# Optimization experiments

Hardware: AMD Instinct MI355X
Metric: run time of the kernel (lower is better)

Reference implementation:

```python
import jax, jax.numpy as jnp
import numpy as np

H = 1024
EPS = 1e-5
MIX_SCALE = 0.1


def setup_inputs() -> dict:
    key = jax.random.key(0)
    ks = jax.random.split(key, 6)
    B, S = 8, 4096
    x = jax.random.normal(ks[0], (B, S, H), dtype=jnp.float32)
    # to_complex: Linear(H, 2H); store weight as [H, 2H] for x @ W
    W_to = jax.random.normal(ks[1], (H, 2 * H), dtype=jnp.float32) * (1.0 / np.sqrt(H))
    b_to = jax.random.normal(ks[2], (2 * H,), dtype=jnp.float32) * 0.01
    # from_complex: Linear(2H, H)
    W_from = jax.random.normal(ks[3], (2 * H, H), dtype=jnp.float32) * (1.0 / np.sqrt(2 * H))
    b_from = jax.random.normal(ks[4], (H,), dtype=jnp.float32) * 0.01
    phase_shifts = jnp.zeros((1, 1, H), dtype=jnp.float32)
    return {"x": x, "W_to": W_to, "b_to": b_to, "W_from": W_from,
            "b_from": b_from, "phase_shifts": phase_shifts}


def reference(x, W_to, b_to, W_from, b_from, phase_shifts):
    # x: [B,S,H]
    complex_repr = x @ W_to + b_to                      # [B,S,2H]
    real, imag = jnp.split(complex_repr, 2, axis=-1)    # each [B,S,H]
    magnitude = jnp.sqrt(real**2 + imag**2 + EPS)
    phase = jnp.arctan2(imag, real)                     # [B,S,H]
    # mean_j cos(phase_i - phase_j + shift)
    #   = cos(phase_i + shift) * mean_j cos(phase_j)
    #   + sin(phase_i + shift) * mean_j sin(phase_j)
    # (exact trig identity; replaces the [B,S,S,H] materialization)
    mean_cos = jnp.mean(jnp.cos(phase), axis=1, keepdims=True)  # [B,1,H]
    mean_sin = jnp.mean(jnp.sin(phase), axis=1, keepdims=True)  # [B,1,H]
    shifted = phase + phase_shifts                              # [B,S,H]
    mixed_phase = jnp.cos(shifted) * mean_cos + jnp.sin(shifted) * mean_sin
    new_phase = phase + mixed_phase * MIX_SCALE
    new_real = magnitude * jnp.cos(new_phase)
    new_imag = magnitude * jnp.sin(new_phase)
    new_complex = jnp.concatenate([new_real, new_imag], axis=-1)  # [B,S,2H]
    return new_complex @ W_from + b_from                          # [B,S,H]
```

## Files before the change

### kernel.cpp

```cpp
#include <hip/hip_runtime.h>
#include <hip/hip_bf16.h>
#include <math.h>

#define H 1024
#define N1 2048
#define BATCH 8
#define SEQ 4096
#define M_TOT (BATCH*SEQ)
#define EPS 1e-5f
#define MIX 0.1f

typedef __attribute__((ext_vector_type(8))) short bf16x8;
typedef __attribute__((ext_vector_type(4))) float f32x4;
typedef unsigned int uint_t;

static __device__ __forceinline__ float bf2f(unsigned short u) {
    return __uint_as_float(((unsigned)u) << 16);
}
static __device__ __forceinline__ unsigned short f2bf(float x) {
    __hip_bfloat16 h = __float2bfloat16(x);
    return *reinterpret_cast<unsigned short*>(&h);
}
static __device__ __forceinline__ void gload16(const void* g, void* l) {
    __builtin_amdgcn_global_load_lds(
        (const __attribute__((address_space(1))) unsigned int*)g,
        (__attribute__((address_space(3))) unsigned int*)l,
        16, 0, 0);
}
static __device__ __forceinline__ int perm2h(int c)  { return ((c & 1023) << 1) | (c >> 10); }

__global__ __launch_bounds__(256) void cvt_f32_bf16(
    const float* __restrict__ in, unsigned short* __restrict__ out, size_t n)
{
    size_t i = ((size_t)blockIdx.x * 256 + threadIdx.x) * 8;
    if (i >= n) return;
    float4 a = *(const float4*)(in + i);
    float4 b = *(const float4*)(in + i + 4);
    union { unsigned short u[8]; uint4 v; } p;
    p.u[0] = f2bf(a.x); p.u[1] = f2bf(a.y); p.u[2] = f2bf(a.z); p.u[3] = f2bf(a.w);
    p.u[4] = f2bf(b.x); p.u[5] = f2bf(b.y); p.u[6] = f2bf(b.z); p.u[7] = f2bf(b.w);
    *(uint4*)(out + i) = p.v;
}

__global__ __launch_bounds__(256) void transpose_wt(
    const float* __restrict__ in, unsigned short* __restrict__ out)
{
    __shared__ float tile[64][65];
    const int c0 = blockIdx.x * 64, r0 = blockIdx.y * 64;
    const int tc = threadIdx.x & 63, tr4 = (threadIdx.x >> 6) * 16;
    #pragma unroll
    for (int rr = 0; rr < 16; ++rr)
        tile[tr4 + rr][tc] = in[(size_t)(r0 + tr4 + rr) * N1 + c0 + tc];
    __syncthreads();
    #pragma unroll
    for (int rr = 0; rr < 16; ++rr)
        out[(size_t)perm2h(c0 + tr4 + rr) * H + r0 + tc] = f2bf(tile[tc][tr4 + rr]);
}

__global__ __launch_bounds__(256) void transpose_wf(
    const float* __restrict__ in, unsigned short* __restrict__ out)
{
    __shared__ float tile[64][65];
    const int n0 = blockIdx.x * 64, k0 = blockIdx.y * 64;
    const int tc = threadIdx.x & 63, tr4 = (threadIdx.x >> 6) * 16;
    #pragma unroll
    for (int rr = 0; rr < 16; ++rr) {
        const int k = k0 + tr4 + rr;
        tile[tr4 + rr][tc] = in[(size_t)((k >> 1) | ((k & 1) << 10)) * H + n0 + tc];
    }
    __syncthreads();
    #pragma unroll
    for (int rr = 0; rr < 16; ++rr)
        out[(size_t)(n0 + tr4 + rr) * N1 + k0 + tc] = f2bf(tile[tc][tr4 + rr]);
}

#define VMW(N) asm volatile("s_waitcnt vmcnt(" #N ")" ::: "memory")
#define SB __builtin_amdgcn_sched_barrier(0)

#define STG(X, BB, HH, CC, TT) \
    gload16(X##g + (size_t)((HH)*128 + (CC)*64) * KDIM + (TT)*64, \
            &X##s[BB][(HH)*8192 + (CC)*4096 + t*8])
#define STAGE_HT(X, BB, HH, TT) do { STG(X, BB, HH, 0, TT); STG(X, BB, HH, 1, TT); } while(0)

#define LDA(BB, MF, KS) (*(const bf16x8*)&As[BB][(wr*128 + (MF)*16 + fr)*64 + ((((KS)*4 + lg) ^ rsw))*8])
#define LDB(BB, NF, KS) (*(const bf16x8*)&Bs[BB][(wc*64  + (NF)*16 + fr)*64 + ((((KS)*4 + lg) ^ rsw))*8])

#define LOADB(BB, KS) do {                                                      \
    _Pragma("unroll")                                                           \
    for (int nf = 0; nf < 4; ++nf) bfr[nf] = LDB(BB, nf, KS); } while (0)
#define LOADA(AN, BB, MFQ, KS) do {                                             \
    _Pragma("unroll")                                                           \
    for (int i = 0; i < 4; ++i) AN[i] = LDA(BB, (MFQ)*4 + i, KS); } while (0)
#define MFMAS(AC, MFQ) do {                                                     \
    _Pragma("unroll")                                                           \
    for (int i = 0; i < 4; ++i)                                                 \
        _Pragma("unroll")                                                       \
        for (int nf = 0; nf < 4; ++nf)                                          \
            acc[(MFQ)*4 + i][nf] = __builtin_amdgcn_mfma_f32_16x16x32_bf16(     \
                AC[i], bfr[nf], acc[(MFQ)*4 + i][nf], 0, 0, 0); } while (0)

#define PH(VMPRE, BLOAD, ALOAD, STAGE_STMT, MFMA_STMT) do {                     \
    VMPRE; SB;                                                                  \
    BLOAD; SB;                                                                  \
    ALOAD; SB;                                                                  \
    STAGE_STMT; SB;                                                             \
    __builtin_amdgcn_s_barrier();                                               \
    asm volatile("s_waitcnt lgkmcnt(4)" ::: "memory");                          \
    SB;                                                                         \
    __builtin_amdgcn_s_setprio(1);                                              \
    MFMA_STMT;                                                                  \
    __builtin_amdgcn_s_setprio(0);                                              \
    __builtin_amdgcn_s_barrier();                                               \
} while (0)

#define NOP ((void)0)

template<int KDIM, bool G1>
__global__ __launch_bounds__(512, 2) void gemm8(
    const unsigned short* __restrict__ A,
    const unsigned short* __restrict__ Bt,
    const float* __restrict__ bias,
    void* __restrict__ Cout,
    float* __restrict__ sums)
{
    __shared__ __align__(16) unsigned short As[2][16384];
    __shared__ __align__(16) unsigned short Bs[2][16384];

    const int t    = threadIdx.x;
    const int lane = t & 63;
    const int wid  = t >> 6;
    const int wr   = wid >> 2;
    const int wc   = wid & 3;

    int m0, n0;
    if (G1) {
        const unsigned wg = ((blockIdx.x & 7) << 7) | (blockIdx.x >> 3);
        n0 = (wg & 7) * 256;
        m0 = (wg >> 3) * 256;
    } else {
        const unsigned wg = ((blockIdx.x & 7) << 6) | (blockIdx.x >> 3);
        n0 = (wg & 3) * 256;
        m0 = (wg >> 2) * 256;
    }

    const int srow = t >> 3;
    const int ssw  = srow & 7;
    const int gk   = ((t & 7) ^ ssw) * 8;
    const unsigned short* Ag = A  + (size_t)(m0 + srow) * KDIM + gk;
    const unsigned short* Bg = Bt + (size_t)(n0 + srow) * KDIM + gk;

    const int fr  = lane & 15;
    const int lg  = lane >> 4;
    const int rsw = fr & 7;

    f32x4 acc[8][4] = {};
    bf16x8 bfr[4];
    bf16x8 aX[4];
    bf16x8 aY[4];

    constexpr int NITER = KDIM / 128;

    STAGE_HT(A, 0, 0, 0); STAGE_HT(A, 0, 1, 0);
    STAGE_HT(B, 0, 0, 0); STAGE_HT(B, 0, 1, 0);
    STAGE_HT(B, 1, 0, 1); STAGE_HT(B, 1, 1, 1);
    VMW(4);
    SB;
    __builtin_amdgcn_s_barrier();
    SB;
    LOADA(aX, 0, 0, 0);
    SB;

    for (int it = 0; it < NITER; ++it) {
        const int  T1   = 2 * it + 1;
        const int  T2   = 2 * it + 2;
        const int  T3   = 2 * it + 3;
        const bool more = (it + 1 < NITER);
        PH(NOP, LOADB(0,0), LOADA(aY,0,1,0), STAGE_HT(A,1,0,T1), MFMAS(aX,0));
        PH(NOP, NOP, LOADA(aX,0,0,1), STAGE_HT(A,1,1,T1), MFMAS(aY,1));
        PH(NOP, LOADB(0,1), LOADA(aY,0,1,1), if (more) STAGE_HT(B,0,0,T2), MFMAS(aX,0));
        PH(if (more) { VMW(2); } else { VMW(0); }, NOP, LOADA(aX,1,0,0),
           if (more) STAGE_HT(B,0,1,T2), MFMAS(aY,1));
        PH(NOP, LOADB(1,0), LOADA(aY,1,1,0), if (more) STAGE_HT(A,0,0,T2), MFMAS(aX,0));
        PH(NOP, NOP, LOADA(aX,1,0,1), if (more) STAGE_HT(A,0,1,T2), MFMAS(aY,1));
        PH(NOP, LOADB(1,1), LOADA(aY,1,1,1), if (more) STAGE_HT(B,1,0,T3), MFMAS(aX,0));
        PH(if (more) { VMW(2); }, NOP, LOADA(aX,0,0,0),
           if (more) STAGE_HT(B,1,1,T3), MFMAS(aY,1));
    }

    const int colbase = n0 + wc * 64;
    if (G1) {
        unsigned short* c1 = (unsigned short*)Cout;
        #pragma unroll
        for (int nf = 0; nf < 4; ++nf) {
            const int col = colbase + nf * 16 + fr;
            const float bb = bias[(col >> 1) | ((col & 1) << 10)];
            #pragma unroll
            for (int mf = 0; mf < 8; ++mf)
                #pragma unroll
                for (int r = 0; r < 4; ++r)
                    acc[mf][nf][r] += bb;
        }
        float lc[4] = {0, 0, 0, 0}, ls[4] = {0, 0, 0, 0};
        #pragma unroll
        for (int nf = 0; nf < 4; ++nf)
            #pragma unroll
            for (int mf = 0; mf < 8; ++mf)
                #pragma unroll
                for (int r = 0; r < 4; ++r) {
                    const float v = acc[mf][nf][r];
                    const float oth = __shfl_xor(v, 1);
                    const float re = (fr & 1) ? oth : v;
                    const float im = (fr & 1) ? v : oth;
                    const float rq = rsqrtf(fmaxf(re * re + im * im, 1e-30f));
                    lc[nf] += re * rq;
                    ls[nf] += im * rq;
                }
        #pragma unroll
        for (int nf = 0; nf < 4; ++nf) {
            lc[nf] += __shfl_xor(lc[nf], 16); lc[nf] += __shfl_xor(lc[nf], 32);
            ls[nf] += __shfl_xor(ls[nf], 16); ls[nf] += __shfl_xor(ls[nf], 32);
        }
        if (lane < 16 && !(lane & 1)) {
            const int b = m0 >> 12;
            #pragma unroll
            for (int nf = 0; nf < 4; ++nf) {
                const int hh = (colbase + nf * 16 + fr) >> 1;
                atomicAdd(&sums[(b * 2 + 0) * H + hh], lc[nf]);
                atomicAdd(&sums[(b * 2 + 1) * H + hh], ls[nf]);
            }
        }
        unsigned short* cst = &As[0][0] + wid * 2048;
        const int row16 = lane >> 2;
        #pragma unroll
        for (int mf = 0; mf < 8; ++mf) {
            #pragma unroll
            for (int nf = 0; nf < 4; ++nf)
                #pragma unroll
                for (int r = 0; r < 4; ++r)
                    cst[(lg * 4 + r) * 68 + nf * 16 + fr] = f2bf(acc[mf][nf][r]);
            const size_t grow = (size_t)(m0 + wr * 128 + mf * 16 + row16);
            #pragma unroll
            for (int c = 0; c < 2; ++c) {
                const int chunk = (lane & 3) + c * 4;
                uint4 v = *(const uint4*)&cst[row16 * 68 + chunk * 8];
                *(uint4*)&c1[grow * N1 + colbase + chunk * 8] = v;
            }
        }
    } else {
        float* o = (float*)Cout;
        #pragma unroll
        for (int nf = 0; nf < 4; ++nf) {
            const int col = colbase + nf * 16 + fr;
            const float bb = bias[col];
            #pragma unroll
            for (int mf = 0; mf < 8; ++mf) {
                #pragma unroll
                for (int r = 0; r < 4; ++r) {
                    const size_t row = (size_t)(m0 + wr * 128 + mf * 16 + lg * 4 + r);
                    o[row * H + col] = acc[mf][nf][r] + bb;
                }
            }
        }
    }
}

__global__ void finalize_pq(const float* __restrict__ sums, const float* __restrict__ ps,
                            float* __restrict__ P, float* __restrict__ Q)
{
    int i = blockIdx.x * 256 + threadIdx.x;
    int b = i >> 10, h = i & (H - 1);
    float mc = sums[(b * 2 + 0) * H + h] * (1.0f / SEQ);
    float ms = sums[(b * 2 + 1) * H + h] * (1.0f / SEQ);
    float cp = cosf(ps[h]), sp = sinf(ps[h]);
    P[i] = mc * cp + ms * sp;
    Q[i] = ms * cp - mc * sp;
}

__global__ __launch_bounds__(256) void phase_mix(
    unsigned short* __restrict__ c1, const float* __restrict__ P,
    const float* __restrict__ Q)
{
    const size_t total = (size_t)M_TOT * N1 / 8;
    for (size_t q = (size_t)blockIdx.x * 256 + threadIdx.x; q < total;
         q += (size_t)gridDim.x * 256) {
        const size_t m = q >> 8;
        const int off = ((int)q & 255) * 8;
        const int b = (int)(m >> 12);
        const int h0 = off >> 1;
        uint4* cu = (uint4*)c1;
        const size_t idx = ((size_t)m * N1 + off) >> 3;
        uint4 v = cu[idx];
        float4 Pv = *(const float4*)&P[b * H + h0];
        float4 Qv = *(const float4*)&Q[b * H + h0];
        const uint_t w[4] = { v.x, v.y, v.z, v.w };
        const float Pk[4] = { Pv.x, Pv.y, Pv.z, Pv.w };
        const float Qk[4] = { Qv.x, Qv.y, Qv.z, Qv.w };
        uint_t o[4];
        #pragma unroll
        for (int e = 0; e < 4; ++e) {
            float r  = bf2f(w[e] & 0xffff);
            float im = bf2f(w[e] >> 16);
            float tt = r * r + im * im;
            float minv = rsqrtf(fmaxf(tt, 1e-30f));
            float d = MIX * (r * Pk[e] + im * Qk[e]) * minv;
            float d2 = d * d;
            float cd = 1.0f - d2 * (0.5f - d2 * (1.0f / 24.0f));
            float sd = d * (1.0f - d2 * ((1.0f / 6.0f) - d2 * (1.0f / 120.0f)));
            float sc = sqrtf(tt + EPS) * minv;
            o[e] = (uint_t)f2bf(sc * (r * cd - im * sd))
                 | ((uint_t)f2bf(sc * (im * cd + r * sd)) << 16);
        }
        v.x = o[0]; v.y = o[1]; v.z = o[2]; v.w = o[3];
        cu[idx] = v;
    }
}

extern "C" void kernel_launch(void* const* d_in, const int* in_sizes, int n_in,
                              void* d_out, int out_size, void* d_ws, size_t ws_size,
                              hipStream_t stream) {
    const float* x  = (const float*)d_in[0];
    const float* Wt = (const float*)d_in[1];
    const float* bt = (const float*)d_in[2];
    const float* Wf = (const float*)d_in[3];
    const float* bf = (const float*)d_in[4];
    const float* ps = (const float*)d_in[5];
    float* out = (float*)d_out;

    const size_t c1_bytes   = (size_t)M_TOT * N1 * 2;
    const size_t wft_bytes  = (size_t)H * N1 * 2;
    const size_t sums_bytes = (size_t)BATCH * 2 * H * 4;
    const size_t pq_bytes   = (size_t)BATCH * H * 4;
    if (ws_size < c1_bytes + wft_bytes + sums_bytes + 2 * pq_bytes) return;

    unsigned short* c1  = (unsigned short*)d_ws;
    unsigned short* WfT = (unsigned short*)((char*)d_ws + c1_bytes);
    float* sums = (float*)((char*)d_ws + c1_bytes + wft_bytes);
    float* Pb   = (float*)((char*)d_ws + c1_bytes + wft_bytes + sums_bytes);
    float* Qb   = (float*)((char*)d_ws + c1_bytes + wft_bytes + sums_bytes + pq_bytes);

    unsigned short* xb  = (unsigned short*)d_out;
    unsigned short* WtT = (unsigned short*)d_out + (size_t)M_TOT * H;

    hipMemsetAsync(sums, 0, sums_bytes, stream);

    cvt_f32_bf16<<<dim3((unsigned)(((size_t)M_TOT * H / 8 + 255) / 256)), 256, 0, stream>>>(
        x, xb, (size_t)M_TOT * H);
    transpose_wt<<<dim3(N1 / 64, H / 64), 256, 0, stream>>>(Wt, WtT);
    transpose_wf<<<dim3(H / 64, N1 / 64), 256, 0, stream>>>(Wf, WfT);

    gemm8<H, true><<<dim3(1024), 512, 0, stream>>>(xb, WtT, bt, (void*)c1, sums);

    finalize_pq<<<dim3(BATCH * H / 256), 256, 0, stream>>>(sums, ps, Pb, Qb);
    phase_mix<<<dim3(4096), 256, 0, stream>>>(c1, Pb, Qb);

    gemm8<N1, false><<<dim3(512), 512, 0, stream>>>(c1, WfT, bf, (void*)out, nullptr);
}
```

Measured before the change: 361.3 us.

## Replace first GEMM with simpler 256x128-tile double-buffered kernel

```diff
diff --git a/kernel.cpp b/kernel.cpp
--- a/kernel.cpp
+++ b/kernel.cpp
@@ -72,6 +72,140 @@
     #pragma unroll
     for (int rr = 0; rr < 16; ++rr)
         out[(size_t)(n0 + tr4 + rr) * N1 + k0 + tc] = f2bf(tile[tc][tr4 + rr]);
+}
+
+__global__ __launch_bounds__(256, 2) void gemm1_2b(
+    const unsigned short* __restrict__ A,
+    const unsigned short* __restrict__ Bt,
+    const float* __restrict__ bt,
+    unsigned short* __restrict__ c1,
+    float* __restrict__ sums)
+{
+    __shared__ __align__(16) unsigned short As[2][8192];
+    __shared__ __align__(16) unsigned short Bs[2][4096];
+
+    const int t    = threadIdx.x;
+    const int lane = t & 63;
+    const int wid  = t >> 6;
+    const int wr   = wid >> 1;
+    const int wc   = wid & 1;
+
+    const unsigned wg = ((blockIdx.x & 7) << 8) | (blockIdx.x >> 3);
+    const int n0 = (wg & 15) * 128;
+    const int m0 = (wg >> 4) * 256;
+
+    const int srow = t >> 2;
+    const int gk   = ((t & 3) ^ ((t >> 3) & 3)) * 8;
+    const unsigned short* Ag = A  + (size_t)(m0 + srow) * H + gk;
+    const unsigned short* Bg = Bt + (size_t)(n0 + srow) * H + gk;
+
+    const int fr  = lane & 15;
+    const int lg  = lane >> 4;
+    const int rsw = (fr >> 1) & 3;
+
+    f32x4 acc[8][4] = {};
+
+    #define STAGE1(b, kt) do {                                                   \
+        _Pragma("unroll")                                                        \
+        for (int c = 0; c < 4; ++c)                                              \
+            gload16(Ag + (size_t)(c * 64) * H + (kt) * 32, &As[b][c * 2048 + t * 8]); \
+        _Pragma("unroll")                                                        \
+        for (int c = 0; c < 2; ++c)                                              \
+            gload16(Bg + (size_t)(c * 64) * H + (kt) * 32, &Bs[b][c * 2048 + t * 8]); \
+    } while (0)
+
+    STAGE1(0, 0);
+    __syncthreads();
+
+    #pragma unroll 2
+    for (int kt = 0; kt < H / 32; ++kt) {
+        const int cur = kt & 1;
+        if (kt + 1 < H / 32) STAGE1(cur ^ 1, kt + 1);
+
+        bf16x8 bfr[4], afr[4];
+        #pragma unroll
+        for (int nf = 0; nf < 4; ++nf)
+            bfr[nf] = *(const bf16x8*)&Bs[cur][(wc * 64 + nf * 16 + fr) * 32 + (lg ^ rsw) * 8];
+        #pragma unroll
+        for (int i = 0; i < 4; ++i)
+            afr[i] = *(const bf16x8*)&As[cur][(wr * 128 + i * 16 + fr) * 32 + (lg ^ rsw) * 8];
+        #pragma unroll
+        for (int i = 0; i < 4; ++i)
+            #pragma unroll
+            for (int nf = 0; nf < 4; ++nf)
+                acc[i][nf] = __builtin_amdgcn_mfma_f32_16x16x32_bf16(
+                    afr[i], bfr[nf], acc[i][nf], 0, 0, 0);
+        #pragma unroll
+        for (int i = 0; i < 4; ++i)
+            afr[i] = *(const bf16x8*)&As[cur][(wr * 128 + (4 + i) * 16 + fr) * 32 + (lg ^ rsw) * 8];
+        #pragma unroll
+        for (int i = 0; i < 4; ++i)
+            #pragma unroll
+            for (int nf = 0; nf < 4; ++nf)
+                acc[4 + i][nf] = __builtin_amdgcn_mfma_f32_16x16x32_bf16(
+                    afr[i], bfr[nf], acc[4 + i][nf], 0, 0, 0);
+
+        __syncthreads();
+    }
+    #undef STAGE1
+
+    const int colbase = n0 + wc * 64;
+    #pragma unroll
+    for (int nf = 0; nf < 4; ++nf) {
+        const int col = colbase + nf * 16 + fr;
+        const float bb = bt[(col >> 1) | ((col & 1) << 10)];
+        #pragma unroll
+        for (int mf = 0; mf < 8; ++mf)
+            #pragma unroll
+            for (int r = 0; r < 4; ++r)
+                acc[mf][nf][r] += bb;
+    }
+    float lc[4] = {0, 0, 0, 0}, ls[4] = {0, 0, 0, 0};
+    #pragma unroll
+    for (int nf = 0; nf < 4; ++nf)
+        #pragma unroll
+        for (int mf = 0; mf < 8; ++mf)
+            #pragma unroll
+            for (int r = 0; r < 4; ++r) {
+                const float v = acc[mf][nf][r];
+                const float oth = __shfl_xor(v, 1);
+                const float re = (fr & 1) ? oth : v;
+                const float im = (fr & 1) ? v : oth;
+                const float rq = rsqrtf(fmaxf(re * re + im * im, 1e-30f));
+                lc[nf] += re * rq;
+                ls[nf] += im * rq;
+            }
+    #pragma unroll
+    for (int nf = 0; nf < 4; ++nf) {
+        lc[nf] += __shfl_xor(lc[nf], 16); lc[nf] += __shfl_xor(lc[nf], 32);
+        ls[nf] += __shfl_xor(ls[nf], 16); ls[nf] += __shfl_xor(ls[nf], 32);
+    }
+    if (lane < 16 && !(lane & 1)) {
+        const int b = m0 >> 12;
+        #pragma unroll
+        for (int nf = 0; nf < 4; ++nf) {
+            const int hh = (colbase + nf * 16 + fr) >> 1;
+            atomicAdd(&sums[(b * 2 + 0) * H + hh], lc[nf]);
+            atomicAdd(&sums[(b * 2 + 1) * H + hh], ls[nf]);
+        }
+    }
+    unsigned short* cst = &As[0][0] + wid * 1088;
+    const int row16 = lane >> 2;
+    #pragma unroll
+    for (int mf = 0; mf < 8; ++mf) {
+        #pragma unroll
+        for (int nf = 0; nf < 4; ++nf)
+            #pragma unroll
+            for (int r = 0; r < 4; ++r)
+                cst[(lg * 4 + r) * 68 + nf * 16 + fr] = f2bf(acc[mf][nf][r]);
+        const size_t grow = (size_t)(m0 + wr * 128 + mf * 16 + row16);
+        #pragma unroll
+        for (int c = 0; c < 2; ++c) {
+            const int chunk = (lane & 3) + c * 4;
+            uint4 v = *(const uint4*)&cst[row16 * 68 + chunk * 8];
+            *(uint4*)&c1[grow * N1 + colbase + chunk * 8] = v;
+        }
+    }
 }
 
 #define VMW(N) asm volatile("s_waitcnt vmcnt(" #N ")" ::: "memory")
@@ -115,13 +249,12 @@
 
 #define NOP ((void)0)
 
-template<int KDIM, bool G1>
+template<int KDIM>
 __global__ __launch_bounds__(512, 2) void gemm8(
     const unsigned short* __restrict__ A,
     const unsigned short* __restrict__ Bt,
     const float* __restrict__ bias,
-    void* __restrict__ Cout,
-    float* __restrict__ sums)
+    float* __restrict__ Cout)
 {
     __shared__ __align__(16) unsigned short As[2][16384];
     __shared__ __align__(16) unsigned short Bs[2][16384];
@@ -132,16 +265,9 @@
     const int wr   = wid >> 2;
     const int wc   = wid & 3;
 
-    int m0, n0;
-    if (G1) {
-        const unsigned wg = ((blockIdx.x & 7) << 7) | (blockIdx.x >> 3);
-        n0 = (wg & 7) * 256;
-        m0 = (wg >> 3) * 256;
-    } else {
-        const unsigned wg = ((blockIdx.x & 7) << 6) | (blockIdx.x >> 3);
-        n0 = (wg & 3) * 256;
-        m0 = (wg >> 2) * 256;
-    }
+    const unsigned wg = ((blockIdx.x & 7) << 6) | (blockIdx.x >> 3);
+    const int n0 = (wg & 3) * 256;
+    const int m0 = (wg >> 2) * 256;
 
     const int srow = t >> 3;
     const int ssw  = srow & 7;
@@ -188,77 +314,17 @@
     }
 
     const int colbase = n0 + wc * 64;
-    if (G1) {
-        unsigned short* c1 = (unsigned short*)Cout;
-        #pragma unroll
-        for (int nf = 0; nf < 4; ++nf) {
-            const int col = colbase + nf * 16 + fr;
-            const float bb = bias[(col >> 1) | ((col & 1) << 10)];
-            #pragma unroll
-            for (int mf = 0; mf < 8; ++mf)
-                #pragma unroll
-                for (int r = 0; r < 4; ++r)
-                    acc[mf][nf][r] += bb;
-        }
-        float lc[4] = {0, 0, 0, 0}, ls[4] = {0, 0, 0, 0};
-        #pragma unroll
-        for (int nf = 0; nf < 4; ++nf)
-            #pragma unroll
-            for (int mf = 0; mf < 8; ++mf)
-                #pragma unroll
-                for (int r = 0; r < 4; ++r) {
-                    const float v = acc[mf][nf][r];
-                    const float oth = __shfl_xor(v, 1);
-                    const float re = (fr & 1) ? oth : v;
-                    const float im = (fr & 1) ? v : oth;
-                    const float rq = rsqrtf(fmaxf(re * re + im * im, 1e-30f));
-                    lc[nf] += re * rq;
-                    ls[nf] += im * rq;
-                }
-        #pragma unroll
-        for (int nf = 0; nf < 4; ++nf) {
-            lc[nf] += __shfl_xor(lc[nf], 16); lc[nf] += __shfl_xor(lc[nf], 32);
-            ls[nf] += __shfl_xor(ls[nf], 16); ls[nf] += __shfl_xor(ls[nf], 32);
-        }
-        if (lane < 16 && !(lane & 1)) {
-            const int b = m0 >> 12;
-            #pragma unroll
-            for (int nf = 0; nf < 4; ++nf) {
-                const int hh = (colbase + nf * 16 + fr) >> 1;
-                atomicAdd(&sums[(b * 2 + 0) * H + hh], lc[nf]);
-                atomicAdd(&sums[(b * 2 + 1) * H + hh], ls[nf]);
-            }
-        }
-        unsigned short* cst = &As[0][0] + wid * 2048;
-        const int row16 = lane >> 2;
+    float* o = Cout;
+    #pragma unroll
+    for (int nf = 0; nf < 4; ++nf) {
+        const int col = colbase + nf * 16 + fr;
+        const float bb = bias[col];
         #pragma unroll
         for (int mf = 0; mf < 8; ++mf) {
             #pragma unroll
-            for (int nf = 0; nf < 4; ++nf)
-                #pragma unroll
-                for (int r = 0; r < 4; ++r)
-                    cst[(lg * 4 + r) * 68 + nf * 16 + fr] = f2bf(acc[mf][nf][r]);
-            const size_t grow = (size_t)(m0 + wr * 128 + mf * 16 + row16);
-            #pragma unroll
-            for (int c = 0; c < 2; ++c) {
-                const int chunk = (lane & 3) + c * 4;
-                uint4 v = *(const uint4*)&cst[row16 * 68 + chunk * 8];
-                *(uint4*)&c1[grow * N1 + colbase + chunk * 8] = v;
-            }
-        }
-    } else {
-        float* o = (float*)Cout;
-        #pragma unroll
-        for (int nf = 0; nf < 4; ++nf) {
-            const int col = colbase + nf * 16 + fr;
-            const float bb = bias[col];
-            #pragma unroll
-            for (int mf = 0; mf < 8; ++mf) {
-                #pragma unroll
-                for (int r = 0; r < 4; ++r) {
-                    const size_t row = (size_t)(m0 + wr * 128 + mf * 16 + lg * 4 + r);
-                    o[row * H + col] = acc[mf][nf][r] + bb;
-                }
+            for (int r = 0; r < 4; ++r) {
+                const size_t row = (size_t)(m0 + wr * 128 + mf * 16 + lg * 4 + r);
+                o[row * H + col] = acc[mf][nf][r] + bb;
             }
         }
     }
@@ -348,10 +414,10 @@
     transpose_wt<<<dim3(N1 / 64, H / 64), 256, 0, stream>>>(Wt, WtT);
     transpose_wf<<<dim3(H / 64, N1 / 64), 256, 0, stream>>>(Wf, WfT);
 
-    gemm8<H, true><<<dim3(1024), 512, 0, stream>>>(xb, WtT, bt, (void*)c1, sums);
+    gemm1_2b<<<dim3(2048), 256, 0, stream>>>(xb, WtT, bt, c1, sums);
 
     finalize_pq<<<dim3(BATCH * H / 256), 256, 0, stream>>>(sums, ps, Pb, Qb);
     phase_mix<<<dim3(4096), 256, 0, stream>>>(c1, Pb, Qb);
 
-    gemm8<N1, false><<<dim3(512), 512, 0, stream>>>(c1, WfT, bf, (void*)out, nullptr);
-}
+    gemm8<N1><<<dim3(512), 512, 0, stream>>>(c1, WfT, bf, out);
+}
```

New measurement: 396.2 us. 1.1x slower.
